# Optimization experiments

Hardware: AMD Instinct MI355X
Metric: run time of the kernel (lower is better)

The kernel has to match this reference:

```python
import jax, jax.numpy as jnp
import numpy as np
from math import sqrt

# Complete K-ary tree: level l has K**l nodes; children of node j at level l
# are nodes j*K .. j*K+K-1 of level l+1. Levels are processed leaves->root.
K = 4
LEVELS = 9
N_NODES = (K ** LEVELS - 1) // (K - 1)  # 87381
X_SIZE = 256
H_SIZE = 256
A_SIZE = 256
N_HEADS = 8
A_K = A_SIZE // N_HEADS


def setup_inputs() -> dict:
    key = jax.random.key(0)
    ks = jax.random.split(key, 20)
    s = 0.02
    d = {
        'x': jax.random.normal(ks[0], (N_NODES, X_SIZE), dtype=jnp.float32),
        'W_iou': jax.random.normal(ks[1], (X_SIZE, 3 * H_SIZE), dtype=jnp.float32) * s,
        'b_iou': jnp.zeros((3 * H_SIZE,), dtype=jnp.float32),
        'W_f': jax.random.normal(ks[2], (X_SIZE, H_SIZE), dtype=jnp.float32) * s,
        'b_f': jnp.zeros((H_SIZE,), dtype=jnp.float32),
        'Wq': jax.random.normal(ks[3], (X_SIZE, A_SIZE), dtype=jnp.float32) * s,
        'bq': jax.random.normal(ks[4], (A_SIZE,), dtype=jnp.float32) * s,
        'Wk': jax.random.normal(ks[5], (H_SIZE, A_SIZE), dtype=jnp.float32) * s,
        'bk': jax.random.normal(ks[6], (A_SIZE,), dtype=jnp.float32) * s,
        'Wv': jax.random.normal(ks[7], (H_SIZE, A_SIZE), dtype=jnp.float32) * s,
        'bv': jax.random.normal(ks[8], (A_SIZE,), dtype=jnp.float32) * s,
        'Wl': jax.random.normal(ks[9], (A_SIZE, A_SIZE), dtype=jnp.float32) * s,
        'bl': jax.random.normal(ks[10], (A_SIZE,), dtype=jnp.float32) * s,
        'Uiou_w': jax.random.normal(ks[11], (A_SIZE, 3 * H_SIZE), dtype=jnp.float32) * s,
        'Uiou_b': jax.random.normal(ks[12], (3 * H_SIZE,), dtype=jnp.float32) * s,
        'Uf_w': jax.random.normal(ks[13], (A_SIZE, H_SIZE), dtype=jnp.float32) * s,
        'Uf_b': jax.random.normal(ks[14], (H_SIZE,), dtype=jnp.float32) * s,
    }
    return d


def _tree_lstm(x, W_iou, b_iou, W_f, b_f, Wq, bq, Wk, bk, Wv, bv, Wl, bl,
               Uiou_w, Uiou_b, Uf_w, Uf_b):
    scale = 1.0 / sqrt(A_K)
    x_iou = x @ W_iou + b_iou          # [N, 3H]
    x_f = x @ W_f + b_f                # [N, H]
    starts = [(K ** l - 1) // (K - 1) for l in range(LEVELS)]
    h_lvl = [None] * LEVELS
    c_lvl = [None] * LEVELS
    for l in reversed(range(LEVELS)):
        s0 = starts[l]
        n = K ** l
        xi = x_iou[s0:s0 + n]
        xf = x_f[s0:s0 + n]
        if l == LEVELS - 1:  # leaves: empty mailbox
            iou = xi
            fc_sum = jnp.zeros((n, H_SIZE), dtype=x.dtype)
        else:
            ch_h = h_lvl[l + 1].reshape(n, K, H_SIZE)  # children mailbox 'h'
            ch_c = c_lvl[l + 1].reshape(n, K, H_SIZE)  # children mailbox 'c'
            q = (x[s0:s0 + n] @ Wq + bq).reshape(n, N_HEADS, A_K)
            kk = (ch_h @ Wk + bk).reshape(n, K, N_HEADS, A_K)
            vv = (ch_h @ Wv + bv).reshape(n, K, N_HEADS, A_K)
            logits = jnp.einsum('nhd,nkhd->nhk', q, kk) * scale
            attn = jax.nn.softmax(logits, axis=-1)
            out = jnp.einsum('nhk,nkhd->nhd', attn, vv).reshape(n, A_SIZE)
            h_attn = out @ Wl + bl
            h_iou = h_attn @ Uiou_w + Uiou_b
            h_f = h_attn @ Uf_w + Uf_b
            f = jax.nn.sigmoid(xf + h_f)[:, None, :]   # same f for all children
            fc_sum = jnp.sum(ch_c * f, axis=1)
            iou = xi + h_iou
        i, o, u = jnp.split(iou, 3, axis=1)
        c_new = jax.nn.sigmoid(i) * jnp.tanh(u) + fc_sum
        h_new = jax.nn.sigmoid(o) * jnp.tanh(c_new)
        h_lvl[l] = h_new
        c_lvl[l] = c_new
    h = jnp.concatenate(h_lvl, axis=0)
    c = jnp.concatenate(c_lvl, axis=0)
    return h, c


def reference(x, W_iou, b_iou, W_f, b_f, Wq, bq, Wk, bk, Wv, bv, Wl, bl,
              Uiou_w, Uiou_b, Uf_w, Uf_b):
    return _tree_lstm(x, W_iou, b_iou, W_f, b_f, Wq, bq, Wk, bk, Wv, bv,
                      Wl, bl, Uiou_w, Uiou_b, Uf_w, Uf_b)
```

## Files before the change

### kernel.cpp

```cpp
#include <hip/hip_runtime.h>
#include <hip/hip_bf16.h>
#include <math.h>

constexpr int LEVELS_ = 9;
constexpr int N_NODES_ = 87381;
constexpr int HS = 256;
constexpr int N_HEADS_ = 8;

typedef __attribute__((ext_vector_type(8))) short bf16x8;
typedef __attribute__((ext_vector_type(4))) float f32x4;
typedef __attribute__((ext_vector_type(4))) float float4v;

__device__ __forceinline__ short f2bf(float f) {
    union { float f; unsigned u; } a; a.f = f;
    unsigned r = (a.u + 0x7fff + ((a.u >> 16) & 1)) >> 16;
    return (short)r;
}
__device__ __forceinline__ float bf2f(short s) {
    union { unsigned u; float f; } a; a.u = ((unsigned)(unsigned short)s) << 16;
    return a.f;
}
__device__ __forceinline__ float sigm(float x) { return 1.f / (1.f + expf(-x)); }

__device__ __forceinline__ void gl_lds16(const short* g, short* l) {
    __builtin_amdgcn_global_load_lds(
        (const __attribute__((address_space(1))) void*)g,
        (__attribute__((address_space(3))) void*)l, 16, 0, 0);
}


__global__ __launch_bounds__(256) void gemm_bf16(
    const short* __restrict__ A, const short* __restrict__ Bt,
    const float* __restrict__ bias, const short* __restrict__ Cadd,
    void* __restrict__ Cout, int M, int N, int Kd, int out_bf16)
{
    __shared__ __align__(16) short smem[2 * 128 * 64];
    short* As = smem;
    short* Bs = smem + 128 * 64;

    const int tid = threadIdx.x;
    const int lane = tid & 63;
    const int w = tid >> 6;
    const int row0 = blockIdx.y * 128;
    const int col0 = blockIdx.x * 128;
    const int wm = (w >> 1) * 64;
    const int wn = (w & 1) * 64;
    const int q = lane >> 4;
    const int mr = lane & 15;

    const int srl = lane >> 3;
    const int scs = ((lane & 7) ^ srl) * 8;

    f32x4 acc[4][4];
    #pragma unroll
    for (int i = 0; i < 4; i++)
        #pragma unroll
        for (int j = 0; j < 4; j++) acc[i][j] = (f32x4){0.f, 0.f, 0.f, 0.f};

    for (int k0 = 0; k0 < Kd; k0 += 64) {
        __syncthreads();
        #pragma unroll
        for (int i = 0; i < 4; ++i) {
            int s = w * 4 + i;
            int r = s * 8 + srl;
            gl_lds16(A + (size_t)(row0 + r) * Kd + k0 + scs, As + s * 512);
            gl_lds16(Bt + (size_t)(col0 + r) * Kd + k0 + scs, Bs + s * 512);
        }
        __syncthreads();
        #pragma unroll
        for (int h = 0; h < 2; ++h) {
            bf16x8 af[4], bfr[4];
            #pragma unroll
            for (int i = 0; i < 4; ++i) {
                int r = wm + i * 16 + mr;
                af[i] = *(const bf16x8*)(As + r * 64 + ((h * 4 + q) ^ (mr & 7)) * 8);
            }
            #pragma unroll
            for (int j = 0; j < 4; ++j) {
                int r = wn + j * 16 + mr;
                bfr[j] = *(const bf16x8*)(Bs + r * 64 + ((h * 4 + q) ^ (mr & 7)) * 8);
            }
            #pragma unroll
            for (int i = 0; i < 4; ++i)
                #pragma unroll
                for (int j = 0; j < 4; ++j)
                    acc[i][j] = __builtin_amdgcn_mfma_f32_16x16x32_bf16(
                        af[i], bfr[j], acc[i][j], 0, 0, 0);
        }
    }

    if (out_bf16) {
        __syncthreads();
        short* Cs = smem;
        #pragma unroll
        for (int j = 0; j < 4; ++j) {
            int col = wn + j * 16 + mr;
            float bv = bias ? bias[col0 + col] : 0.f;
            #pragma unroll
            for (int i = 0; i < 4; ++i) {
                #pragma unroll
                for (int r = 0; r < 4; ++r) {
                    int lr = wm + i * 16 + q * 4 + r;
                    float v = acc[i][j][r] + bv;
                    if (Cadd && row0 + lr < M)
                        v += bf2f(Cadd[(size_t)(row0 + lr) * N + col0 + col]);
                    Cs[lr * 128 + col] = f2bf(v);
                }
            }
        }
        __syncthreads();
        #pragma unroll
        for (int i = 0; i < 8; ++i) {
            int chunk = i * 256 + tid;
            int lr = chunk >> 4;
            int c8 = (chunk & 15) * 8;
            if (row0 + lr < M)
                *(bf16x8*)((short*)Cout + (size_t)(row0 + lr) * N + col0 + c8) =
                    *(const bf16x8*)(Cs + lr * 128 + c8);
        }
    } else {
        #pragma unroll
        for (int j = 0; j < 4; ++j) {
            int col = col0 + wn + j * 16 + mr;
            float bv = bias ? bias[col] : 0.f;
            #pragma unroll
            for (int i = 0; i < 4; ++i) {
                #pragma unroll
                for (int r = 0; r < 4; ++r) {
                    int grow = row0 + wm + i * 16 + q * 4 + r;
                    if (grow < M) {
                        size_t off = (size_t)grow * N + col;
                        float v = acc[i][j][r] + bv;
                        if (Cadd) v += bf2f(Cadd[off]);
                        ((float*)Cout)[off] = v;
                    }
                }
            }
        }
    }
}

__global__ __launch_bounds__(256) void gemm_cell(
    const short* __restrict__ A, const short* __restrict__ Bt,
    const float* __restrict__ bias, const short* __restrict__ Cadd,
    const float* __restrict__ c_child,
    float* __restrict__ h_out, float* __restrict__ c_out,
    short* __restrict__ hb_out, int M)
{
    __shared__ __align__(16) short smem[128 * 136];
    short* As = smem;
    short* Bs = smem + 128 * 64;

    const int tid = threadIdx.x;
    const int lane = tid & 63;
    const int w = tid >> 6;
    const int row0 = blockIdx.y * 128;
    const int col0 = blockIdx.x * 128;
    const int wm = (w >> 1) * 64;
    const int wn = (w & 1) * 64;
    const int q = lane >> 4;
    const int mr = lane & 15;

    const int srl = lane >> 3;
    const int scs = ((lane & 7) ^ srl) * 8;

    f32x4 acc[4][4];
    #pragma unroll
    for (int i = 0; i < 4; i++)
        #pragma unroll
        for (int j = 0; j < 4; j++) acc[i][j] = (f32x4){0.f, 0.f, 0.f, 0.f};

    for (int k0 = 0; k0 < 256; k0 += 64) {
        __syncthreads();
        #pragma unroll
        for (int i = 0; i < 4; ++i) {
            int s = w * 4 + i;
            int r = s * 8 + srl;
            gl_lds16(A + (size_t)(row0 + r) * 256 + k0 + scs, As + s * 512);
            gl_lds16(Bt + (size_t)(col0 + r) * 256 + k0 + scs, Bs + s * 512);
        }
        __syncthreads();
        #pragma unroll
        for (int h = 0; h < 2; ++h) {
            bf16x8 af[4], bfr[4];
            #pragma unroll
            for (int i = 0; i < 4; ++i) {
                int r = wm + i * 16 + mr;
                af[i] = *(const bf16x8*)(As + r * 64 + ((h * 4 + q) ^ (mr & 7)) * 8);
            }
            #pragma unroll
            for (int j = 0; j < 4; ++j) {
                int r = wn + j * 16 + mr;
                bfr[j] = *(const bf16x8*)(Bs + r * 64 + ((h * 4 + q) ^ (mr & 7)) * 8);
            }
            #pragma unroll
            for (int i = 0; i < 4; ++i)
                #pragma unroll
                for (int j = 0; j < 4; ++j)
                    acc[i][j] = __builtin_amdgcn_mfma_f32_16x16x32_bf16(
                        af[i], bfr[j], acc[i][j], 0, 0, 0);
        }
    }

    __syncthreads();
    short* Cs = smem;
    #pragma unroll
    for (int j = 0; j < 4; ++j) {
        int col = wn + j * 16 + mr;
        float bv = bias[col0 + col];
        #pragma unroll
        for (int i = 0; i < 4; ++i) {
            #pragma unroll
            for (int r = 0; r < 4; ++r) {
                int lr = wm + i * 16 + q * 4 + r;
                float v = acc[i][j][r] + bv;
                if (Cadd && row0 + lr < M)
                    v += bf2f(Cadd[(size_t)(row0 + lr) * 1024 + col0 + col]);
                Cs[lr * 136 + col] = f2bf(v);
            }
        }
    }
    __syncthreads();

    const int hd0 = blockIdx.x * 32;
    #pragma unroll 1
    for (int it = 0; it < 2; ++it) {
        int chunk = it * 256 + tid;
        int row = chunk >> 2;
        int d8 = (chunk & 3) * 8;
        int gp = row0 + row;
        if (gp < M) {
            bf16x8 vi = *(const bf16x8*)(Cs + row * 136 + d8);
            bf16x8 vo = *(const bf16x8*)(Cs + row * 136 + 32 + d8);
            bf16x8 vu = *(const bf16x8*)(Cs + row * 136 + 64 + d8);
            float fc[8] = {0.f, 0.f, 0.f, 0.f, 0.f, 0.f, 0.f, 0.f};
            if (c_child) {
                bf16x8 vf = *(const bf16x8*)(Cs + row * 136 + 96 + d8);
                #pragma unroll
                for (int c = 0; c < 4; ++c) {
                    const float* cp = c_child + (size_t)(4 * gp + c) * 256 + hd0 + d8;
                    float4v a = *(const float4v*)cp;
                    float4v b = *(const float4v*)(cp + 4);
                    #pragma unroll
                    for (int e = 0; e < 4; ++e) { fc[e] += a[e]; fc[4 + e] += b[e]; }
                }
                #pragma unroll
                for (int e = 0; e < 8; ++e) fc[e] *= sigm(bf2f(vf[e]));
            }
            float4v hv[2], cv[2];
            bf16x8 hbv;
            #pragma unroll
            for (int e = 0; e < 8; ++e) {
                float cn = sigm(bf2f(vi[e])) * tanhf(bf2f(vu[e])) + fc[e];
                float hn = sigm(bf2f(vo[e])) * tanhf(cn);
                hv[e >> 2][e & 3] = hn;
                cv[e >> 2][e & 3] = cn;
                hbv[e] = f2bf(hn);
            }
            size_t o = (size_t)gp * 256 + hd0 + d8;
            *(float4v*)(h_out + o) = hv[0]; *(float4v*)(h_out + o + 4) = hv[1];
            *(float4v*)(c_out + o) = cv[0]; *(float4v*)(c_out + o + 4) = cv[1];
            *(bf16x8*)(hb_out + o) = hbv;
        }
    }
}

__global__ __launch_bounds__(256) void kv_attn(
    const short* __restrict__ A,
    const short* __restrict__ B3t,
    const float* __restrict__ bias_kv,
    const short* __restrict__ qb_lvl,
    short* __restrict__ outb)
{
    __shared__ __align__(16) short smem[2 * 128 * 64 + 32 * 64];
    short* As = smem;
    short* Bs = smem + 128 * 64;
    short* sh_o = smem + 2 * 128 * 64;

    const int tid = threadIdx.x;
    const int lane = tid & 63;
    const int w = tid >> 6;
    const int row0 = blockIdx.y * 128;
    const int colb = blockIdx.x;
    const int col0 = colb * 128;
    const int wm = (w >> 1) * 64;
    const int wn = (w & 1) * 64;
    const int q = lane >> 4;
    const int mr = lane & 15;

    const int srl = lane >> 3;
    const int scs = ((lane & 7) ^ srl) * 8;

    f32x4 acc[4][4];
    #pragma unroll
    for (int i = 0; i < 4; i++)
        #pragma unroll
        for (int j = 0; j < 4; j++) acc[i][j] = (f32x4){0.f, 0.f, 0.f, 0.f};

    for (int k0 = 0; k0 < 256; k0 += 64) {
        __syncthreads();
        #pragma unroll
        for (int i = 0; i < 4; ++i) {
            int s = w * 4 + i;
            int r = s * 8 + srl;
            gl_lds16(A + (size_t)(row0 + r) * 256 + k0 + scs, As + s * 512);
            gl_lds16(B3t + (size_t)(col0 + r) * 256 + k0 + scs, Bs + s * 512);
        }
        __syncthreads();
        #pragma unroll
        for (int h = 0; h < 2; ++h) {
            bf16x8 af[4], bfr[4];
            #pragma unroll
            for (int i = 0; i < 4; ++i) {
                int r = wm + i * 16 + mr;
                af[i] = *(const bf16x8*)(As + r * 64 + ((h * 4 + q) ^ (mr & 7)) * 8);
            }
            #pragma unroll
            for (int j = 0; j < 4; ++j) {
                int r = wn + j * 16 + mr;
                bfr[j] = *(const bf16x8*)(Bs + r * 64 + ((h * 4 + q) ^ (mr & 7)) * 8);
            }
            #pragma unroll
            for (int i = 0; i < 4; ++i)
                #pragma unroll
                for (int j = 0; j < 4; ++j)
                    acc[i][j] = __builtin_amdgcn_mfma_f32_16x16x32_bf16(
                        af[i], bfr[j], acc[i][j], 0, 0, 0);
        }
    }

    __syncthreads();
    short* Cs = smem;
    #pragma unroll
    for (int j = 0; j < 4; ++j) {
        int col = wn + j * 16 + mr;
        float bv = bias_kv[col0 + col];
        #pragma unroll
        for (int i = 0; i < 4; ++i) {
            #pragma unroll
            for (int r = 0; r < 4; ++r) {
                int lr = wm + i * 16 + q * 4 + r;
                Cs[lr * 128 + col] = f2bf(acc[i][j][r] + bv);
            }
        }
    }
    __syncthreads();

    const int p0 = blockIdx.y * 32;
    const int grp0 = tid >> 5;
    const int l32 = tid & 31;
    #pragma unroll 1
    for (int it = 0; it < 8; ++it) {
        int pair = it * 8 + grp0;
        int pl = pair >> 1, hh = pair & 1;
        float qv = bf2f(qb_lvl[(size_t)(p0 + pl) * 256 + (colb * 2 + hh) * 32 + l32]);
        float logit[4];
        #pragma unroll
        for (int c = 0; c < 4; ++c) {
            float pch = qv * bf2f(Cs[(4 * pl + c) * 128 + hh * 64 + l32]);
            #pragma unroll
            for (int off = 16; off >= 1; off >>= 1)
                pch += __shfl_xor(pch, off, 32);
            logit[c] = pch * 0.17677669529663687f;
        }
        float mx = fmaxf(fmaxf(logit[0], logit[1]), fmaxf(logit[2], logit[3]));
        float e[4], s = 0.f;
        #pragma unroll
        for (int c = 0; c < 4; ++c) { e[c] = expf(logit[c] - mx); s += e[c]; }
        float inv = 1.f / s;
        float o = 0.f;
        #pragma unroll
        for (int c = 0; c < 4; ++c)
            o += (e[c] * inv) * bf2f(Cs[(4 * pl + c) * 128 + hh * 64 + 32 + l32]);
        sh_o[pl * 64 + hh * 32 + l32] = f2bf(o);
    }
    __syncthreads();
    {
        int r = tid >> 3, c8 = (tid & 7) * 8;
        *(bf16x8*)(outb + (size_t)(p0 + r) * 256 + colb * 64 + c8) =
            *(const bf16x8*)(sh_o + r * 64 + c8);
    }
}

__global__ __launch_bounds__(256) void level_fused(
    const short* __restrict__ hb, const float* __restrict__ c_all,
    const short* __restrict__ qb, const short* __restrict__ xi,
    const short* __restrict__ B3t, const short* __restrict__ Wlt,
    const short* __restrict__ Bt2,
    const float* __restrict__ bias_kv, const float* __restrict__ bl,
    const float* __restrict__ biasU,
    float* __restrict__ h_all, float* __restrict__ c_out_g,
    short* __restrict__ hb_out, int s0, int sc, int n)
{
    __shared__ __align__(16) char smem[50176];
    short* sh_h    = (short*)smem;
    short* sh_kv   = (short*)(smem + 16896);
    short* sh_out  = (short*)smem;
    short* sh_ha   = (short*)(smem + 8448);
    float* sh_iouf = (float*)(smem + 16896);

    const int tid = threadIdx.x;
    const int lane = tid & 63;
    const int w = tid >> 6;
    const int q = lane >> 4;
    const int mr = lane & 15;
    const int p0 = blockIdx.x * 8;
    const int np = (n - p0 < 8) ? (n - p0) : 8;
    const int nch = 4 * np;

    #pragma unroll
    for (int i = 0; i < 4; ++i) {
        int chunk = i * 256 + tid;
        int r = chunk >> 5;
        int c8 = (chunk & 31) * 8;
        bf16x8 v = {};
        if (r < nch) v = *(const bf16x8*)(hb + (size_t)(sc + 4 * p0 + r) * 256 + c8);
        *(bf16x8*)(sh_h + r * 264 + c8) = v;
    }
    __syncthreads();

    {
        f32x4 acc[2][8];
        #pragma unroll
        for (int rt = 0; rt < 2; ++rt)
            #pragma unroll
            for (int ct = 0; ct < 8; ++ct) acc[rt][ct] = (f32x4){0.f, 0.f, 0.f, 0.f};
        #pragma unroll 1
        for (int k0 = 0; k0 < 256; k0 += 32) {
            bf16x8 a0 = *(const bf16x8*)(sh_h + mr * 264 + k0 + q * 8);
            bf16x8 a1 = *(const bf16x8*)(sh_h + (16 + mr) * 264 + k0 + q * 8);
            #pragma unroll
            for (int ct = 0; ct < 8; ++ct) {
                int col = w * 128 + ct * 16 + mr;
                bf16x8 b = *(const bf16x8*)(B3t + (size_t)col * 256 + k0 + q * 8);
                acc[0][ct] = __builtin_amdgcn_mfma_f32_16x16x32_bf16(a0, b, acc[0][ct], 0, 0, 0);
                acc[1][ct] = __builtin_amdgcn_mfma_f32_16x16x32_bf16(a1, b, acc[1][ct], 0, 0, 0);
            }
        }
        #pragma unroll
        for (int ct = 0; ct < 8; ++ct) {
            int col = w * 128 + ct * 16 + mr;
            float bv = bias_kv[col];
            #pragma unroll
            for (int rt = 0; rt < 2; ++rt)
                #pragma unroll
                for (int r = 0; r < 4; ++r) {
                    int row = rt * 16 + q * 4 + r;
                    sh_kv[row * 520 + col] = f2bf(acc[rt][ct][r] + bv);
                }
        }
    }
    __syncthreads();

    {
        const int grp0 = tid >> 5;
        const int l32 = tid & 31;
        #pragma unroll 1
        for (int it = 0; it < 8; ++it) {
            int grp = it * 8 + grp0;
            int node = grp >> 3, head = grp & 7;
            if (node < np) {
                float qv = bf2f(qb[(size_t)(s0 + p0 + node) * 256 + head * 32 + l32]);
                float logit[4];
                #pragma unroll
                for (int c = 0; c < 4; ++c) {
                    float p = qv * bf2f(sh_kv[(4 * node + c) * 520 + head * 64 + l32]);
                    #pragma unroll
                    for (int off = 16; off >= 1; off >>= 1)
                        p += __shfl_xor(p, off, 32);
                    logit[c] = p * 0.17677669529663687f;
                }
                float mx = fmaxf(fmaxf(logit[0], logit[1]), fmaxf(logit[2], logit[3]));
                float e[4], s = 0.f;
                #pragma unroll
                for (int c = 0; c < 4; ++c) { e[c] = expf(logit[c] - mx); s += e[c]; }
                float inv = 1.f / s;
                float o = 0.f;
                #pragma unroll
                for (int c = 0; c < 4; ++c)
                    o += (e[c] * inv) * bf2f(sh_kv[(4 * node + c) * 520 + head * 64 + 32 + l32]);
                sh_out[node * 264 + head * 32 + l32] = f2bf(o);
            }
        }
    }
    __syncthreads();

    {
        f32x4 acc[4];
        #pragma unroll
        for (int ct = 0; ct < 4; ++ct) acc[ct] = (f32x4){0.f, 0.f, 0.f, 0.f};
        #pragma unroll 1
        for (int k0 = 0; k0 < 256; k0 += 32) {
            bf16x8 a = *(const bf16x8*)(sh_out + mr * 264 + k0 + q * 8);
            #pragma unroll
            for (int ct = 0; ct < 4; ++ct) {
                int col = w * 64 + ct * 16 + mr;
                bf16x8 b = *(const bf16x8*)(Wlt + (size_t)col * 256 + k0 + q * 8);
                acc[ct] = __builtin_amdgcn_mfma_f32_16x16x32_bf16(a, b, acc[ct], 0, 0, 0);
            }
        }
        #pragma unroll
        for (int ct = 0; ct < 4; ++ct) {
            int col = w * 64 + ct * 16 + mr;
            float bv = bl[col];
            #pragma unroll
            for (int r = 0; r < 4; ++r) {
                int row = q * 4 + r;
                if (row < np) sh_ha[row * 264 + col] = f2bf(acc[ct][r] + bv);
            }
        }
    }
    __syncthreads();

    {
        f32x4 acc[16];
        #pragma unroll
        for (int ct = 0; ct < 16; ++ct) acc[ct] = (f32x4){0.f, 0.f, 0.f, 0.f};
        #pragma unroll 1
        for (int k0 = 0; k0 < 256; k0 += 32) {
            bf16x8 a = *(const bf16x8*)(sh_ha + mr * 264 + k0 + q * 8);
            #pragma unroll
            for (int ct = 0; ct < 16; ++ct) {
                int col = w * 256 + ct * 16 + mr;
                bf16x8 b = *(const bf16x8*)(Bt2 + (size_t)col * 256 + k0 + q * 8);
                acc[ct] = __builtin_amdgcn_mfma_f32_16x16x32_bf16(a, b, acc[ct], 0, 0, 0);
            }
        }
        __syncthreads();
        #pragma unroll
        for (int ct = 0; ct < 16; ++ct) {
            int col = w * 256 + ct * 16 + mr;
            float bU = biasU[col];
            #pragma unroll
            for (int r = 0; r < 4; ++r) {
                int row = q * 4 + r;
                if (row < np)
                    sh_iouf[row * 1024 + col] =
                        acc[ct][r] + bU + bf2f(xi[(size_t)(s0 + p0 + row) * 1024 + col]);
            }
        }
    }
    __syncthreads();

    #pragma unroll 1
    for (int it = 0; it < 8; ++it) {
        int t = it * 256 + tid;
        if (t < np * 256) {
            int node = t >> 8, j = t & 255;
            int gcol = (j >> 5) * 128 + (j & 31);
            float iv = sh_iouf[node * 1024 + gcol];
            float ov = sh_iouf[node * 1024 + gcol + 32];
            float uv = sh_iouf[node * 1024 + gcol + 64];
            float fv = sigm(sh_iouf[node * 1024 + gcol + 96]);
            float fc = 0.f;
            #pragma unroll
            for (int c = 0; c < 4; ++c)
                fc += c_all[(size_t)(sc + 4 * (p0 + node) + c) * 256 + j] * fv;
            float cn = sigm(iv) * tanhf(uv) + fc;
            float hn = sigm(ov) * tanhf(cn);
            size_t o = (size_t)(s0 + p0 + node) * 256 + j;
            h_all[o] = hn;
            c_out_g[o] = cn;
            hb_out[o] = f2bf(hn);
        }
    }
}

__global__ __launch_bounds__(256) void conv_x(
    const float* __restrict__ x, short* __restrict__ xb, int n8)
{
    int t = blockIdx.x * 256 + threadIdx.x;
    if (t >= n8) return;
    float4v a = *(const float4v*)(x + (size_t)t * 8);
    float4v b = *(const float4v*)(x + (size_t)t * 8 + 4);
    bf16x8 o;
    o[0] = f2bf(a.x); o[1] = f2bf(a.y); o[2] = f2bf(a.z); o[3] = f2bf(a.w);
    o[4] = f2bf(b.x); o[5] = f2bf(b.y); o[6] = f2bf(b.z); o[7] = f2bf(b.w);
    *(bf16x8*)(xb + (size_t)t * 8) = o;
}

__global__ __launch_bounds__(256) void prep_weights(
    const float* __restrict__ W_iou, const float* __restrict__ W_f,
    const float* __restrict__ Uiou_w, const float* __restrict__ Uf_w,
    const float* __restrict__ Wk, const float* __restrict__ Wv,
    const float* __restrict__ Wq, const float* __restrict__ Wl,
    const float* __restrict__ b_iou, const float* __restrict__ b_f,
    const float* __restrict__ Uiou_b, const float* __restrict__ Uf_b,
    const float* __restrict__ bk, const float* __restrict__ bv,
    short* __restrict__ Bt1, short* __restrict__ Bt2, short* __restrict__ B3t,
    short* __restrict__ Wqt, short* __restrict__ Wlt,
    float* __restrict__ biasX, float* __restrict__ biasU,
    float* __restrict__ bias_kv)
{
    int t = blockIdx.x * 256 + threadIdx.x;
    if (t < 262144) {
        int gc = t >> 8, k = t & 255;
        int within = gc & 127, gate = within >> 5, d = (gc >> 7) * 32 + (within & 31);
        float v = (gate < 3) ? W_iou[k * 768 + gate * 256 + d] : W_f[k * 256 + d];
        Bt1[t] = f2bf(v);
        return;
    }
    t -= 262144;
    if (t < 262144) {
        int gc = t >> 8, k = t & 255;
        int within = gc & 127, gate = within >> 5, d = (gc >> 7) * 32 + (within & 31);
        float v = (gate < 3) ? Uiou_w[k * 768 + gate * 256 + d] : Uf_w[k * 256 + d];
        Bt2[t] = f2bf(v);
        return;
    }
    t -= 262144;
    if (t < 131072) {
        int gc = t >> 8, k = t & 255;
        int head = gc >> 6, kv = (gc >> 5) & 1, d = head * 32 + (gc & 31);
        float v = kv ? Wv[k * 256 + d] : Wk[k * 256 + d];
        B3t[t] = f2bf(v);
        return;
    }
    t -= 131072;
    if (t < 65536) { int nn = t >> 8, k = t & 255; Wqt[t] = f2bf(Wq[k * 256 + nn]); return; }
    t -= 65536;
    if (t < 65536) { int nn = t >> 8, k = t & 255; Wlt[t] = f2bf(Wl[k * 256 + nn]); return; }
    t -= 65536;
    if (t < 1024) {
        int within = t & 127, gate = within >> 5, d = (t >> 7) * 32 + (within & 31);
        biasX[t] = (gate < 3) ? b_iou[gate * 256 + d] : b_f[d];
        return;
    }
    t -= 1024;
    if (t < 1024) {
        int within = t & 127, gate = within >> 5, d = (t >> 7) * 32 + (within & 31);
        biasU[t] = (gate < 3) ? Uiou_b[gate * 256 + d] : Uf_b[d];
        return;
    }
    t -= 1024;
    if (t < 512) {
        int head = t >> 6, kv = (t >> 5) & 1, d = head * 32 + (t & 31);
        bias_kv[t] = kv ? bv[d] : bk[d];
        return;
    }
}

static inline void launch_gemm(const short* A, const short* Bt, const float* bias,
                               const short* Cadd, void* C, int M, int N, int Kd,
                               int out_bf16, hipStream_t stream)
{
    dim3 grid(N / 128, (M + 127) / 128);
    gemm_bf16<<<grid, 256, 0, stream>>>(A, Bt, bias, Cadd, C, M, N, Kd, out_bf16);
}

extern "C" void kernel_launch(void* const* d_in, const int* in_sizes, int n_in,
                              void* d_out, int out_size, void* d_ws, size_t ws_size,
                              hipStream_t stream)
{
    const float* x      = (const float*)d_in[0];
    const float* W_iou  = (const float*)d_in[1];
    const float* b_iou  = (const float*)d_in[2];
    const float* W_f    = (const float*)d_in[3];
    const float* b_f    = (const float*)d_in[4];
    const float* Wq     = (const float*)d_in[5];
    const float* bq     = (const float*)d_in[6];
    const float* Wk     = (const float*)d_in[7];
    const float* bk     = (const float*)d_in[8];
    const float* Wv     = (const float*)d_in[9];
    const float* bv     = (const float*)d_in[10];
    const float* Wl     = (const float*)d_in[11];
    const float* bl     = (const float*)d_in[12];
    const float* Uiou_w = (const float*)d_in[13];
    const float* Uiou_b = (const float*)d_in[14];
    const float* Uf_w   = (const float*)d_in[15];
    const float* Uf_b   = (const float*)d_in[16];

    float* h_all = (float*)d_out;
    float* c_all = h_all + (size_t)N_NODES_ * HS;

    char* p = (char*)d_ws;
    short* xb   = (short*)p; p += (size_t)N_NODES_ * 256 * 2;
    short* hb   = (short*)p; p += (size_t)N_NODES_ * 256 * 2;
    short* xi   = (short*)p; p += (size_t)21845 * 1024 * 2;
    short* qb   = (short*)p; p += (size_t)21845 * 256 * 2;
    short* outb = (short*)p; p += (size_t)16384 * 256 * 2;
    short* hab  = (short*)p; p += (size_t)16384 * 256 * 2;
    short* Bt1  = (short*)p; p += (size_t)1024 * 256 * 2;
    short* Bt2  = (short*)p; p += (size_t)1024 * 256 * 2;
    short* B3t  = (short*)p; p += (size_t)512 * 256 * 2;
    short* Wqt  = (short*)p; p += (size_t)256 * 256 * 2;
    short* Wlt  = (short*)p; p += (size_t)256 * 256 * 2;
    float* biasX   = (float*)p; p += 1024 * 4;
    float* biasU   = (float*)p; p += 1024 * 4;
    float* bias_kv = (float*)p; p += 512 * 4;

    static const int starts[LEVELS_] = {0, 1, 5, 21, 85, 341, 1365, 5461, 21845};

    {
        int n8 = N_NODES_ * 256 / 8;
        conv_x<<<(n8 + 255) / 256, 256, 0, stream>>>(x, xb, n8);
        int total = 262144 + 262144 + 131072 + 65536 + 65536 + 1024 + 1024 + 512;
        prep_weights<<<(total + 255) / 256, 256, 0, stream>>>(
            W_iou, W_f, Uiou_w, Uf_w, Wk, Wv, Wq, Wl,
            b_iou, b_f, Uiou_b, Uf_b, bk, bv,
            Bt1, Bt2, B3t, Wqt, Wlt, biasX, biasU, bias_kv);
    }

    launch_gemm(xb, Bt1, biasX, nullptr, xi, 21845, 1024, 256, 1, stream);
    launch_gemm(xb, Wqt, bq, nullptr, qb, 21845, 256, 256, 1, stream);

    {
        dim3 grid(8, 65536 / 128);
        gemm_cell<<<grid, 256, 0, stream>>>(
            xb + (size_t)21845 * 256, Bt1, biasX, nullptr, nullptr,
            h_all + (size_t)21845 * HS, c_all + (size_t)21845 * HS,
            hb + (size_t)21845 * HS, 65536);
    }

    for (int l = 7; l >= 6; l--) {
        int n  = 1 << (2 * l);
        int s0 = starts[l];
        int sc = starts[l + 1];
        int nc = 4 * n;

        dim3 gkv(4, nc / 128);
        kv_attn<<<gkv, 256, 0, stream>>>(
            hb + (size_t)sc * 256, B3t, bias_kv, qb + (size_t)s0 * 256, outb);
        launch_gemm(outb, Wlt, bl, nullptr, hab, n, 256, 256, 1, stream);
        dim3 gc(8, n / 128);
        gemm_cell<<<gc, 256, 0, stream>>>(
            hab, Bt2, biasU, xi + (size_t)s0 * 1024, c_all + (size_t)sc * HS,
            h_all + (size_t)s0 * HS, c_all + (size_t)s0 * HS,
            hb + (size_t)s0 * HS, n);
    }

    for (int l = 5; l >= 0; l--) {
        int n  = 1 << (2 * l);
        int s0 = starts[l];
        int sc = starts[l + 1];
        int blocks = (n + 7) / 8;
        level_fused<<<blocks, 256, 0, stream>>>(
            hb, c_all, qb, xi, B3t, Wlt, Bt2, bias_kv, bl, biasU,
            h_all, c_all, hb, s0, sc, n);
    }
}
```

Before: 880.3 us.

## Fuse Q projection into x GEMM, swizzle blocks across XCDs, skip leaf forget MFMAs

Several unrelated changes are combined. The x->iou GEMM and the x->q GEMM become one launch over 1280 output columns by placing Wqt next to Bt1 and splitting the output into xi and qb. All GEMM-style kernels remap block IDs so that consecutive tiles land on the same XCD, which targets L2 reuse. Leaf-level gemm_cell skips loading and computing the forget-gate columns, which leaves do not need. expf/tanhf are replaced with fast __expf-based versions, trading some accuracy for fewer instructions.

```diff
diff --git a/kernel.cpp b/kernel.cpp
--- a/kernel.cpp
+++ b/kernel.cpp
@@ -20,7 +20,12 @@
     union { unsigned u; float f; } a; a.u = ((unsigned)(unsigned short)s) << 16;
     return a.f;
 }
-__device__ __forceinline__ float sigm(float x) { return 1.f / (1.f + expf(-x)); }
+__device__ __forceinline__ float sigm(float x) { return 1.f / (1.f + __expf(-x)); }
+__device__ __forceinline__ float ftanh(float x) {
+    float e = __expf(-2.f * fabsf(x));
+    float t = (1.f - e) / (1.f + e);
+    return copysignf(t, x);
+}
 
 __device__ __forceinline__ void gl_lds16(const short* g, short* l) {
     __builtin_amdgcn_global_load_lds(
@@ -28,11 +33,18 @@
         (__attribute__((address_space(3))) void*)l, 16, 0, 0);
 }
 
+__device__ __forceinline__ int xcd_swizzle(int flat, int nwg) {
+    int q = nwg >> 3, r = nwg & 7;
+    int xcd = flat & 7, idx = flat >> 3;
+    int base = (xcd < r) ? xcd * (q + 1) : r * (q + 1) + (xcd - r) * q;
+    return base + idx;
+}
 
 __global__ __launch_bounds__(256) void gemm_bf16(
     const short* __restrict__ A, const short* __restrict__ Bt,
     const float* __restrict__ bias, const short* __restrict__ Cadd,
-    void* __restrict__ Cout, int M, int N, int Kd, int out_bf16)
+    void* __restrict__ Cout, int M, int N, int Kd, int out_bf16,
+    short* __restrict__ Cout2, int Nsplit)
 {
     __shared__ __align__(16) short smem[2 * 128 * 64];
     short* As = smem;
@@ -41,8 +53,10 @@
     const int tid = threadIdx.x;
     const int lane = tid & 63;
     const int w = tid >> 6;
-    const int row0 = blockIdx.y * 128;
-    const int col0 = blockIdx.x * 128;
+    const int gx = gridDim.x;
+    const int sw = xcd_swizzle(blockIdx.y * gx + blockIdx.x, gx * gridDim.y);
+    const int row0 = (sw / gx) * 128;
+    const int col0 = (sw % gx) * 128;
     const int wm = (w >> 1) * 64;
     const int wn = (w & 1) * 64;
     const int q = lane >> 4;
@@ -89,6 +103,11 @@
         }
     }
 
+    short* dst;
+    int width, colbase;
+    if (Cout2 && col0 >= Nsplit) { dst = Cout2; colbase = col0 - Nsplit; width = N - Nsplit; }
+    else { dst = (short*)Cout; colbase = col0; width = Cout2 ? Nsplit : N; }
+
     if (out_bf16) {
         __syncthreads();
         short* Cs = smem;
@@ -103,7 +122,7 @@
                     int lr = wm + i * 16 + q * 4 + r;
                     float v = acc[i][j][r] + bv;
                     if (Cadd && row0 + lr < M)
-                        v += bf2f(Cadd[(size_t)(row0 + lr) * N + col0 + col]);
+                        v += bf2f(Cadd[(size_t)(row0 + lr) * width + colbase + col]);
                     Cs[lr * 128 + col] = f2bf(v);
                 }
             }
@@ -115,7 +134,7 @@
             int lr = chunk >> 4;
             int c8 = (chunk & 15) * 8;
             if (row0 + lr < M)
-                *(bf16x8*)((short*)Cout + (size_t)(row0 + lr) * N + col0 + c8) =
+                *(bf16x8*)(dst + (size_t)(row0 + lr) * width + colbase + c8) =
                     *(const bf16x8*)(Cs + lr * 128 + c8);
         }
     } else {
@@ -154,8 +173,11 @@
     const int tid = threadIdx.x;
     const int lane = tid & 63;
     const int w = tid >> 6;
-    const int row0 = blockIdx.y * 128;
-    const int col0 = blockIdx.x * 128;
+    const int gx = gridDim.x;
+    const int sw = xcd_swizzle(blockIdx.y * gx + blockIdx.x, gx * gridDim.y);
+    const int row0 = (sw / gx) * 128;
+    const int bxs = sw % gx;
+    const int col0 = bxs * 128;
     const int wm = (w >> 1) * 64;
     const int wn = (w & 1) * 64;
     const int q = lane >> 4;
@@ -164,6 +186,9 @@
     const int srl = lane >> 3;
     const int scs = ((lane & 7) ^ srl) * 8;
 
+    const bool leaf = (c_child == nullptr);
+    const int jn = (leaf && wn == 64) ? 2 : 4;
+
     f32x4 acc[4][4];
     #pragma unroll
     for (int i = 0; i < 4; i++)
@@ -177,7 +202,8 @@
             int s = w * 4 + i;
             int r = s * 8 + srl;
             gl_lds16(A + (size_t)(row0 + r) * 256 + k0 + scs, As + s * 512);
-            gl_lds16(Bt + (size_t)(col0 + r) * 256 + k0 + scs, Bs + s * 512);
+            if (!(leaf && s >= 12))
+                gl_lds16(Bt + (size_t)(col0 + r) * 256 + k0 + scs, Bs + s * 512);
         }
         __syncthreads();
         #pragma unroll
@@ -189,16 +215,18 @@
                 af[i] = *(const bf16x8*)(As + r * 64 + ((h * 4 + q) ^ (mr & 7)) * 8);
             }
             #pragma unroll
-            for (int j = 0; j < 4; ++j) {
-                int r = wn + j * 16 + mr;
-                bfr[j] = *(const bf16x8*)(Bs + r * 64 + ((h * 4 + q) ^ (mr & 7)) * 8);
-            }
+            for (int j = 0; j < 4; ++j)
+                if (j < jn) {
+                    int r = wn + j * 16 + mr;
+                    bfr[j] = *(const bf16x8*)(Bs + r * 64 + ((h * 4 + q) ^ (mr & 7)) * 8);
+                }
             #pragma unroll
             for (int i = 0; i < 4; ++i)
                 #pragma unroll
                 for (int j = 0; j < 4; ++j)
-                    acc[i][j] = __builtin_amdgcn_mfma_f32_16x16x32_bf16(
-                        af[i], bfr[j], acc[i][j], 0, 0, 0);
+                    if (j < jn)
+                        acc[i][j] = __builtin_amdgcn_mfma_f32_16x16x32_bf16(
+                            af[i], bfr[j], acc[i][j], 0, 0, 0);
         }
     }
 
@@ -222,7 +250,7 @@
     }
     __syncthreads();
 
-    const int hd0 = blockIdx.x * 32;
+    const int hd0 = bxs * 32;
     #pragma unroll 1
     for (int it = 0; it < 2; ++it) {
         int chunk = it * 256 + tid;
@@ -234,7 +262,7 @@
             bf16x8 vo = *(const bf16x8*)(Cs + row * 136 + 32 + d8);
             bf16x8 vu = *(const bf16x8*)(Cs + row * 136 + 64 + d8);
             float fc[8] = {0.f, 0.f, 0.f, 0.f, 0.f, 0.f, 0.f, 0.f};
-            if (c_child) {
+            if (!leaf) {
                 bf16x8 vf = *(const bf16x8*)(Cs + row * 136 + 96 + d8);
                 #pragma unroll
                 for (int c = 0; c < 4; ++c) {
@@ -251,8 +279,8 @@
             bf16x8 hbv;
             #pragma unroll
             for (int e = 0; e < 8; ++e) {
-                float cn = sigm(bf2f(vi[e])) * tanhf(bf2f(vu[e])) + fc[e];
-                float hn = sigm(bf2f(vo[e])) * tanhf(cn);
+                float cn = sigm(bf2f(vi[e])) * ftanh(bf2f(vu[e])) + fc[e];
+                float hn = sigm(bf2f(vo[e])) * ftanh(cn);
                 hv[e >> 2][e & 3] = hn;
                 cv[e >> 2][e & 3] = cn;
                 hbv[e] = f2bf(hn);
@@ -280,8 +308,11 @@
     const int tid = threadIdx.x;
     const int lane = tid & 63;
     const int w = tid >> 6;
-    const int row0 = blockIdx.y * 128;
-    const int colb = blockIdx.x;
+    const int gx = gridDim.x;
+    const int sw = xcd_swizzle(blockIdx.y * gx + blockIdx.x, gx * gridDim.y);
+    const int byq = sw / gx;
+    const int colb = sw % gx;
+    const int row0 = byq * 128;
     const int col0 = colb * 128;
     const int wm = (w >> 1) * 64;
     const int wn = (w & 1) * 64;
@@ -346,7 +377,7 @@
     }
     __syncthreads();
 
-    const int p0 = blockIdx.y * 32;
+    const int p0 = byq * 32;
     const int grp0 = tid >> 5;
     const int l32 = tid & 31;
     #pragma unroll 1
@@ -366,7 +397,7 @@
         float mx = fmaxf(fmaxf(logit[0], logit[1]), fmaxf(logit[2], logit[3]));
         float e[4], s = 0.f;
         #pragma unroll
-        for (int c = 0; c < 4; ++c) { e[c] = expf(logit[c] - mx); s += e[c]; }
+        for (int c = 0; c < 4; ++c) { e[c] = __expf(logit[c] - mx); s += e[c]; }
         float inv = 1.f / s;
         float o = 0.f;
         #pragma unroll
@@ -473,7 +504,7 @@
                 float mx = fmaxf(fmaxf(logit[0], logit[1]), fmaxf(logit[2], logit[3]));
                 float e[4], s = 0.f;
                 #pragma unroll
-                for (int c = 0; c < 4; ++c) { e[c] = expf(logit[c] - mx); s += e[c]; }
+                for (int c = 0; c < 4; ++c) { e[c] = __expf(logit[c] - mx); s += e[c]; }
                 float inv = 1.f / s;
                 float o = 0.f;
                 #pragma unroll
@@ -556,8 +587,8 @@
             #pragma unroll
             for (int c = 0; c < 4; ++c)
                 fc += c_all[(size_t)(sc + 4 * (p0 + node) + c) * 256 + j] * fv;
-            float cn = sigm(iv) * tanhf(uv) + fc;
-            float hn = sigm(ov) * tanhf(cn);
+            float cn = sigm(iv) * ftanh(uv) + fc;
+            float hn = sigm(ov) * ftanh(cn);
             size_t o = (size_t)(s0 + p0 + node) * 256 + j;
             h_all[o] = hn;
             c_out_g[o] = cn;
@@ -587,6 +618,7 @@
     const float* __restrict__ b_iou, const float* __restrict__ b_f,
     const float* __restrict__ Uiou_b, const float* __restrict__ Uf_b,
     const float* __restrict__ bk, const float* __restrict__ bv,
+    const float* __restrict__ bq,
     short* __restrict__ Bt1, short* __restrict__ Bt2, short* __restrict__ B3t,
     short* __restrict__ Wqt, short* __restrict__ Wlt,
     float* __restrict__ biasX, float* __restrict__ biasU,
@@ -627,6 +659,8 @@
         return;
     }
     t -= 1024;
+    if (t < 256) { biasX[1024 + t] = bq[t]; return; }
+    t -= 256;
     if (t < 1024) {
         int within = t & 127, gate = within >> 5, d = (t >> 7) * 32 + (within & 31);
         biasU[t] = (gate < 3) ? Uiou_b[gate * 256 + d] : Uf_b[d];
@@ -642,10 +676,11 @@
 
 static inline void launch_gemm(const short* A, const short* Bt, const float* bias,
                                const short* Cadd, void* C, int M, int N, int Kd,
-                               int out_bf16, hipStream_t stream)
+                               int out_bf16, short* C2, int Nsplit, hipStream_t stream)
 {
     dim3 grid(N / 128, (M + 127) / 128);
-    gemm_bf16<<<grid, 256, 0, stream>>>(A, Bt, bias, Cadd, C, M, N, Kd, out_bf16);
+    gemm_bf16<<<grid, 256, 0, stream>>>(A, Bt, bias, Cadd, C, M, N, Kd, out_bf16,
+                                        C2, Nsplit);
 }
 
 extern "C" void kernel_launch(void* const* d_in, const int* in_sizes, int n_in,
@@ -681,11 +716,11 @@
     short* outb = (short*)p; p += (size_t)16384 * 256 * 2;
     short* hab  = (short*)p; p += (size_t)16384 * 256 * 2;
     short* Bt1  = (short*)p; p += (size_t)1024 * 256 * 2;
+    short* Wqt  = (short*)p; p += (size_t)256 * 256 * 2;
     short* Bt2  = (short*)p; p += (size_t)1024 * 256 * 2;
     short* B3t  = (short*)p; p += (size_t)512 * 256 * 2;
-    short* Wqt  = (short*)p; p += (size_t)256 * 256 * 2;
     short* Wlt  = (short*)p; p += (size_t)256 * 256 * 2;
-    float* biasX   = (float*)p; p += 1024 * 4;
+    float* biasX   = (float*)p; p += 1280 * 4;
     float* biasU   = (float*)p; p += 1024 * 4;
     float* bias_kv = (float*)p; p += 512 * 4;
 
@@ -694,15 +729,14 @@
     {
         int n8 = N_NODES_ * 256 / 8;
         conv_x<<<(n8 + 255) / 256, 256, 0, stream>>>(x, xb, n8);
-        int total = 262144 + 262144 + 131072 + 65536 + 65536 + 1024 + 1024 + 512;
+        int total = 262144 + 262144 + 131072 + 65536 + 65536 + 1024 + 256 + 1024 + 512;
         prep_weights<<<(total + 255) / 256, 256, 0, stream>>>(
             W_iou, W_f, Uiou_w, Uf_w, Wk, Wv, Wq, Wl,
-            b_iou, b_f, Uiou_b, Uf_b, bk, bv,
+            b_iou, b_f, Uiou_b, Uf_b, bk, bv, bq,
             Bt1, Bt2, B3t, Wqt, Wlt, biasX, biasU, bias_kv);
     }
 
-    launch_gemm(xb, Bt1, biasX, nullptr, xi, 21845, 1024, 256, 1, stream);
-    launch_gemm(xb, Wqt, bq, nullptr, qb, 21845, 256, 256, 1, stream);
+    launch_gemm(xb, Bt1, biasX, nullptr, xi, 21845, 1280, 256, 1, qb, 1024, stream);
 
     {
         dim3 grid(8, 65536 / 128);
@@ -721,7 +755,7 @@
         dim3 gkv(4, nc / 128);
         kv_attn<<<gkv, 256, 0, stream>>>(
             hb + (size_t)sc * 256, B3t, bias_kv, qb + (size_t)s0 * 256, outb);
-        launch_gemm(outb, Wlt, bl, nullptr, hab, n, 256, 256, 1, stream);
+        launch_gemm(outb, Wlt, bl, nullptr, hab, n, 256, 256, 1, nullptr, 0, stream);
         dim3 gc(8, n / 128);
         gemm_cell<<<gc, 256, 0, stream>>>(
             hab, Bt2, biasU, xi + (size_t)s0 * 1024, c_all + (size_t)sc * HS,
```

Measured after the change: 848.9 us. -3.6%, faster.
